# Kernel optimization log

Measured on AMD Instinct MI355X. Metric: run time of the kernel, lower is better.

## Reference

```python
import jax, jax.numpy as jnp
import numpy as np

B, C, Ci, N = 4, 512, 256, 4096
EPS = 1e-5

def _proj(x, W, b):
    # 1x1 Conv1d == per-node linear: x [B,C,N], W [O,C], b [O] -> [B,O,N]
    return jnp.einsum('oc,bcn->bon', W, x) + b[None, :, None]

def setup_inputs() -> dict:
    key = jax.random.key(0)
    ks = jax.random.split(key, 12)
    s_in = 1.0 / np.sqrt(C)
    s_ci = 1.0 / np.sqrt(Ci)
    return {
        'v':   jax.random.normal(ks[0], (B, C, N), jnp.float32),
        'Wg':  jax.random.normal(ks[1], (Ci, C), jnp.float32) * s_in,
        'bg':  jax.random.normal(ks[2], (Ci,), jnp.float32) * 0.01,
        'Wth': jax.random.normal(ks[3], (Ci, C), jnp.float32) * s_in,
        'bth': jax.random.normal(ks[4], (Ci,), jnp.float32) * 0.01,
        'Wph': jax.random.normal(ks[5], (Ci, C), jnp.float32) * s_in,
        'bph': jax.random.normal(ks[6], (Ci,), jnp.float32) * 0.01,
        'Ww':  jax.random.normal(ks[7], (C, Ci), jnp.float32) * s_ci,
        'bw':  jax.random.normal(ks[8], (C,), jnp.float32) * 0.01,
        'gamma': jax.random.uniform(ks[9], (C,), jnp.float32, 0.5, 1.5),
        'beta':  jax.random.normal(ks[10], (C,), jnp.float32) * 0.01,
    }

def reference(v, Wg, bg, Wth, bth, Wph, bph, Ww, bw, gamma, beta):
    # projections (1x1 convs)
    g_v = _proj(v, Wg, bg).transpose(0, 2, 1)      # [B,N,Ci]
    theta_v = _proj(v, Wth, bth).transpose(0, 2, 1)  # [B,N,Ci]
    phi_v = _proj(v, Wph, bph)                      # [B,Ci,N]
    # non-local affinity (no softmax), divided by N
    R = jnp.einsum('bnc,bcm->bnm', theta_v, phi_v) / N  # [B,N,N]
    y = jnp.einsum('bnm,bmc->bnc', R, g_v)              # [B,N,Ci]
    y = y.transpose(0, 2, 1)                            # [B,Ci,N]
    # W: 1x1 conv back to C, then BatchNorm1d (training-mode stats)
    Wy = _proj(y, Ww, bw)                               # [B,C,N]
    mean = jnp.mean(Wy, axis=(0, 2), keepdims=True)
    var = jnp.mean(jnp.square(Wy - mean), axis=(0, 2), keepdims=True)  # biased, as torch BN uses
    Wy_bn = (Wy - mean) * jax.lax.rsqrt(var + EPS)
    Wy_bn = Wy_bn * gamma[None, :, None] + beta[None, :, None]
    return Wy_bn + v
```

## Files before the change

kernel.cpp:

```cpp
#include <hip/hip_runtime.h>
#include <math.h>


#define B_  4
#define C_  512
#define CI_ 256
#define N_  4096

typedef __attribute__((ext_vector_type(8))) short bf16x8;
typedef __attribute__((ext_vector_type(4))) float f32x4;

#define G_OFF     0L
#define P1_OFF    1048576L
#define SP_OFF    1572864L
#define P2_OFF    1835008L
#define MISC_OFF  2359296L
#define R_OFF     (MISC_OFF + 0)
#define SUM_OFF   (MISC_OFF + 2048)
#define SSQ_OFF   (MISC_OFF + 2560)
#define BE_OFF    (MISC_OFF + 3072)
#define U1_OFF    (MISC_OFF + 5120)
#define U2_OFF    (MISC_OFF + 6144)
#define VH_OFF    2367488L
#define VL_OFF    6561792L
#define VTH_OFF   10756096L
#define WEH_OFF   14950400L
#define WEL_OFF   15474688L

__device__ __forceinline__ unsigned short f2bf(float f) {
    union { float f; unsigned int u; } a; a.f = f;
    unsigned int u = a.u;
    u += 0x7fffu + ((u >> 16) & 1u);
    return (unsigned short)(u >> 16);
}
__device__ __forceinline__ float bf2f(unsigned short s) {
    union { unsigned int u; float f; } a; a.u = ((unsigned int)s) << 16; return a.f;
}
__device__ __forceinline__ void gload_lds16(const char* g, char* l) {
    __builtin_amdgcn_global_load_lds(
        (const __attribute__((address_space(1))) unsigned int*)g,
        (__attribute__((address_space(3))) unsigned int*)l, 16, 0, 0);
}

__global__ __launch_bounds__(256) void cast_fused(
    const float* __restrict__ v, unsigned short* __restrict__ vh,
    unsigned short* __restrict__ vl, unsigned short* __restrict__ vth,
    float* __restrict__ r)
{
    __shared__ float tile[64][65];
    const int b = blockIdx.z;
    const int n0 = blockIdx.x * 64, c0 = blockIdx.y * 64;
    const int t = threadIdx.x, rq = t >> 4, cq = t & 15;
#pragma unroll
    for (int p = 0; p < 4; ++p) {
        int row = p * 16 + rq;
        long e = ((long)(b * C_ + c0 + row)) * N_ + n0 + cq * 4;
        float4 f = *(const float4*)&v[e];
        ushort4 h, l;
        h.x = f2bf(f.x); l.x = f2bf(f.x - bf2f(h.x));
        h.y = f2bf(f.y); l.y = f2bf(f.y - bf2f(h.y));
        h.z = f2bf(f.z); l.z = f2bf(f.z - bf2f(h.z));
        h.w = f2bf(f.w); l.w = f2bf(f.w - bf2f(h.w));
        *(ushort4*)&vh[e] = h;
        *(ushort4*)&vl[e] = l;
        tile[row][cq * 4 + 0] = f.x; tile[row][cq * 4 + 1] = f.y;
        tile[row][cq * 4 + 2] = f.z; tile[row][cq * 4 + 3] = f.w;
        float s = f.x + f.y + f.z + f.w;
        s += __shfl_xor(s, 1); s += __shfl_xor(s, 2);
        s += __shfl_xor(s, 4); s += __shfl_xor(s, 8);
        if (cq == 0) atomicAdd(&r[b * C_ + c0 + row], s);
    }
    __syncthreads();
#pragma unroll
    for (int p = 0; p < 4; ++p) {
        int nl = p * 16 + rq;
        float f0 = tile[cq * 4 + 0][nl], f1 = tile[cq * 4 + 1][nl];
        float f2 = tile[cq * 4 + 2][nl], f3 = tile[cq * 4 + 3][nl];
        ushort4 h;
        h.x = f2bf(f0); h.y = f2bf(f1); h.z = f2bf(f2); h.w = f2bf(f3);
        long e = ((long)(b * N_ + n0 + nl)) * C_ + c0 + cq * 4;
        *(ushort4*)&vth[e] = h;
    }
}

__global__ __launch_bounds__(256, 4) void gram_mfma(
    const unsigned short* __restrict__ vh, const unsigned short* __restrict__ vl,
    float* __restrict__ G)
{
    __shared__ char smem[32768];
    const int t = threadIdx.x, lane = t & 63, w = t >> 6;
    const int z = blockIdx.z, b = z >> 3, ch = z & 7;
    const long m0 = blockIdx.y * 128, n0 = blockIdx.x * 64;
    const long k0b = (long)ch * 1024;
    const long stride = (long)N_ * 2;

    const char* g; char* lbase;
    if (w == 0)      { g = (const char*)(vh + ((long)b * C_ + m0     ) * N_) + k0b; lbase = smem; }
    else if (w == 1) { g = (const char*)(vh + ((long)b * C_ + m0 + 64) * N_) + k0b; lbase = smem + 8192; }
    else if (w == 2) { g = (const char*)(vh + ((long)b * C_ + n0     ) * N_) + k0b; lbase = smem + 16384; }
    else             { g = (const char*)(vl + ((long)b * C_ + n0     ) * N_) + k0b; lbase = smem + 24576; }
    const char* gs = g + (long)(lane >> 3) * stride + (((lane & 7) ^ (lane >> 3)) << 4);

    const int wr = w >> 1, wc = w & 1;
    const int l15 = lane & 15, hi4 = lane >> 4;
    const int swz = (l15 & 7) << 4;
    const int arow = (wr * 64 + l15) * 128;
    const int brow = (wc * 32 + l15) * 128;
    const char* Ah = smem;
    const char* Bh = smem + 16384;
    const char* Bl = smem + 24576;

    f32x4 acc[4][2];
#pragma unroll
    for (int mi = 0; mi < 4; ++mi)
#pragma unroll
        for (int nj = 0; nj < 2; ++nj) acc[mi][nj] = (f32x4){0.f, 0.f, 0.f, 0.f};

    for (int s = 0; s < 8; ++s) {
#pragma unroll
        for (int i = 0; i < 8; ++i)
            gload_lds16(gs + (long)i * 8 * stride + s * 128, lbase + i * 1024);
        __syncthreads();
#pragma unroll
        for (int kk = 0; kk < 2; ++kk) {
            const int off = (kk * 64 + hi4 * 16) ^ swz;
            bf16x8 ah[4], bh[2], bl[2];
#pragma unroll
            for (int mi = 0; mi < 4; ++mi)
                ah[mi] = *(const bf16x8*)(Ah + arow + mi * 2048 + off);
#pragma unroll
            for (int nj = 0; nj < 2; ++nj) {
                bh[nj] = *(const bf16x8*)(Bh + brow + nj * 2048 + off);
                bl[nj] = *(const bf16x8*)(Bl + brow + nj * 2048 + off);
            }
#pragma unroll
            for (int mi = 0; mi < 4; ++mi)
#pragma unroll
                for (int nj = 0; nj < 2; ++nj)
                    acc[mi][nj] = __builtin_amdgcn_mfma_f32_16x16x32_bf16(ah[mi], bh[nj], acc[mi][nj], 0, 0, 0);
#pragma unroll
            for (int mi = 0; mi < 4; ++mi)
#pragma unroll
                for (int nj = 0; nj < 2; ++nj)
                    acc[mi][nj] = __builtin_amdgcn_mfma_f32_16x16x32_bf16(ah[mi], bl[nj], acc[mi][nj], 0, 0, 0);
        }
        __syncthreads();
    }
#pragma unroll
    for (int mi = 0; mi < 4; ++mi)
#pragma unroll
        for (int nj = 0; nj < 2; ++nj)
#pragma unroll
            for (int rr = 0; rr < 4; ++rr) {
                long row = m0 + wr * 64 + mi * 16 + hi4 * 4 + rr;
                long col = n0 + wc * 32 + nj * 16 + l15;
                atomicAdd(&G[((long)b * C_ + row) * C_ + col], acc[mi][nj][rr]);
            }
}

__global__ __launch_bounds__(256, 4) void wy_mfma(
    const unsigned short* __restrict__ weh, const unsigned short* __restrict__ wel,
    const unsigned short* __restrict__ vth,
    const float* __restrict__ be, const float* __restrict__ bw,
    float* __restrict__ out, float* __restrict__ sums, float* __restrict__ ssqs)
{
    __shared__ char smem[40960];
    const int t = threadIdx.x, lane = t & 63, w = t >> 6;
    const int b = blockIdx.z;
    const long m0 = blockIdx.y * 128;
    const long n0 = blockIdx.x * 64;
    const long S = (long)C_ * 2;

    const char* wehb = (const char*)(weh + ((long)b * C_ + m0) * C_);
    const char* welb = (const char*)(wel + ((long)b * C_ + m0) * C_);
    const char* vhb  = (const char*)(vth + ((long)b * N_ + n0) * C_);

    const char *g0, *g1; char *l0, *l1; int c0n;
    if (w == 0)      { g0 = wehb;           l0 = smem;                 c0n = 10; g1 = wehb; l1 = smem; }
    else if (w == 1) { g0 = wehb + 80 * S;  l0 = smem + 10240;         c0n = 6;  g1 = welb;          l1 = smem + 16384; }
    else if (w == 2) { g0 = welb + 32 * S;  l0 = smem + 16384 + 4096;  c0n = 10; g1 = welb; l1 = smem + 16384; }
    else             { g0 = welb + 112 * S; l0 = smem + 16384 + 14336; c0n = 2;  g1 = vhb;           l1 = smem + 32768; }
    const long plane = (long)(lane >> 3) * S + (((lane & 7) ^ (lane >> 3)) << 4);

    const int wr = w >> 1, wc = w & 1;
    const int l15 = lane & 15, hi4 = lane >> 4;
    const int swz = (l15 & 7) << 4;
    const int arow = (wr * 64 + l15) * 128;
    const int brow = (wc * 32 + l15) * 128;
    const char* Ah = smem;
    const char* Al = smem + 16384;
    const char* Bv = smem + 32768;

    f32x4 acc[4][2];
#pragma unroll
    for (int mi = 0; mi < 4; ++mi)
#pragma unroll
        for (int nj = 0; nj < 2; ++nj) acc[mi][nj] = (f32x4){0.f, 0.f, 0.f, 0.f};

    for (int s = 0; s < 8; ++s) {
#pragma unroll
        for (int i = 0; i < 10; ++i) {
            const char* src; char* dst;
            if (i < c0n) { src = g0 + (long)i * 8 * S;         dst = l0 + i * 1024; }
            else         { src = g1 + (long)(i - c0n) * 8 * S; dst = l1 + (i - c0n) * 1024; }
            gload_lds16(src + plane + s * 128, dst);
        }
        __syncthreads();
#pragma unroll
        for (int kk = 0; kk < 2; ++kk) {
            const int off = (kk * 64 + hi4 * 16) ^ swz;
            bf16x8 ah[4], al[4], bv[2];
#pragma unroll
            for (int mi = 0; mi < 4; ++mi) {
                ah[mi] = *(const bf16x8*)(Ah + arow + mi * 2048 + off);
                al[mi] = *(const bf16x8*)(Al + arow + mi * 2048 + off);
            }
#pragma unroll
            for (int nj = 0; nj < 2; ++nj)
                bv[nj] = *(const bf16x8*)(Bv + brow + nj * 2048 + off);
#pragma unroll
            for (int mi = 0; mi < 4; ++mi)
#pragma unroll
                for (int nj = 0; nj < 2; ++nj)
                    acc[mi][nj] = __builtin_amdgcn_mfma_f32_16x16x32_bf16(ah[mi], bv[nj], acc[mi][nj], 0, 0, 0);
#pragma unroll
            for (int mi = 0; mi < 4; ++mi)
#pragma unroll
                for (int nj = 0; nj < 2; ++nj)
                    acc[mi][nj] = __builtin_amdgcn_mfma_f32_16x16x32_bf16(al[mi], bv[nj], acc[mi][nj], 0, 0, 0);
        }
        __syncthreads();
    }

    float sm[4][4], sq[4][4];
#pragma unroll
    for (int mi = 0; mi < 4; ++mi)
#pragma unroll
        for (int rr = 0; rr < 4; ++rr) { sm[mi][rr] = 0.f; sq[mi][rr] = 0.f; }

#pragma unroll
    for (int mi = 0; mi < 4; ++mi) {
#pragma unroll
        for (int rr = 0; rr < 4; ++rr) {
            long o = m0 + wr * 64 + mi * 16 + hi4 * 4 + rr;
            float bv = be[b * C_ + o] * (1.0f / (float)N_) + bw[o];
#pragma unroll
            for (int nj = 0; nj < 2; ++nj) {
                long n = n0 + wc * 32 + nj * 16 + l15;
                float val = acc[mi][nj][rr] + bv;
                out[((long)b * C_ + o) * N_ + n] = val;
                sm[mi][rr] += val;
                sq[mi][rr] += val * val;
            }
        }
    }
#pragma unroll
    for (int mi = 0; mi < 4; ++mi)
#pragma unroll
        for (int rr = 0; rr < 4; ++rr) {
            float s1 = sm[mi][rr], s2 = sq[mi][rr];
            s1 += __shfl_xor(s1, 1); s2 += __shfl_xor(s2, 1);
            s1 += __shfl_xor(s1, 2); s2 += __shfl_xor(s2, 2);
            s1 += __shfl_xor(s1, 4); s2 += __shfl_xor(s2, 4);
            s1 += __shfl_xor(s1, 8); s2 += __shfl_xor(s2, 8);
            if (l15 == 0) {
                long o = m0 + wr * 64 + mi * 16 + hi4 * 4 + rr;
                atomicAdd(&sums[o], s1);
                atomicAdd(&ssqs[o], s2);
            }
        }
}

__global__ __launch_bounds__(256) void gemm_nn(
    const float* __restrict__ A, long sA, int lda,
    const float* __restrict__ Bm, long sB, int ldb,
    float* __restrict__ Cm, long sC, int ldc,
    int K, float scale, int mode,
    const float* __restrict__ bth, float* __restrict__ be,
    unsigned short* __restrict__ weh, unsigned short* __restrict__ wel)
{
    int b = blockIdx.z;
    const float* Ab = A + (long)b * sA;
    const float* Bb = Bm + (long)b * sB;
    int i0 = blockIdx.y * 64, j0 = blockIdx.x * 64;

    __shared__ __align__(16) float As[16][64];
    __shared__ __align__(16) float Bs[16][64];

    int t = threadIdx.x, tx = t & 15, ty = t >> 4;
    int am = t >> 2, akq = (t & 3) << 2;
    int bk = t >> 4, bn4 = (t & 15) << 2;

    float acc[4][4];
#pragma unroll
    for (int r = 0; r < 4; ++r)
#pragma unroll
        for (int c = 0; c < 4; ++c) acc[r][c] = 0.f;

    for (int k0 = 0; k0 < K; k0 += 16) {
        float4 va = *(const float4*)&Ab[(long)(i0 + am) * lda + k0 + akq];
        As[akq + 0][am] = va.x; As[akq + 1][am] = va.y;
        As[akq + 2][am] = va.z; As[akq + 3][am] = va.w;
        *(float4*)&Bs[bk][bn4] = *(const float4*)&Bb[(long)(k0 + bk) * ldb + j0 + bn4];
        __syncthreads();
#pragma unroll
        for (int k = 0; k < 16; ++k) {
            float4 a4 = *(float4*)&As[k][ty * 4];
            float4 b4 = *(float4*)&Bs[k][tx * 4];
            float a[4]  = {a4.x, a4.y, a4.z, a4.w};
            float bb[4] = {b4.x, b4.y, b4.z, b4.w};
#pragma unroll
            for (int r = 0; r < 4; ++r)
#pragma unroll
                for (int c = 0; c < 4; ++c)
                    acc[r][c] += a[r] * bb[c];
        }
        __syncthreads();
    }

    if (mode == 2) {
#pragma unroll
        for (int r = 0; r < 4; ++r) {
            int o = i0 + ty * 4 + r, p = j0 + tx * 4;
            ushort4 h, l;
            float f0 = acc[r][0] * scale, f1 = acc[r][1] * scale;
            float f2 = acc[r][2] * scale, f3 = acc[r][3] * scale;
            h.x = f2bf(f0); l.x = f2bf(f0 - bf2f(h.x));
            h.y = f2bf(f1); l.y = f2bf(f1 - bf2f(h.y));
            h.z = f2bf(f2); l.z = f2bf(f2 - bf2f(h.z));
            h.w = f2bf(f3); l.w = f2bf(f3 - bf2f(h.w));
            long e = (((long)b * C_ + o) * C_ + p) >> 2;
            ((ushort4*)weh)[e] = h;
            ((ushort4*)wel)[e] = l;
        }
        return;
    }
    float* Cb = Cm + (long)b * sC;
#pragma unroll
    for (int r = 0; r < 4; ++r) {
        float4 o0 = make_float4(acc[r][0] * scale, acc[r][1] * scale,
                                acc[r][2] * scale, acc[r][3] * scale);
        *(float4*)&Cb[(long)(i0 + ty * 4 + r) * ldc + j0 + tx * 4] = o0;
    }
    if (mode == 1) {
#pragma unroll
        for (int r = 0; r < 4; ++r) {
            float pr = acc[r][0] * bth[j0 + tx * 4 + 0]
                     + acc[r][1] * bth[j0 + tx * 4 + 1]
                     + acc[r][2] * bth[j0 + tx * 4 + 2]
                     + acc[r][3] * bth[j0 + tx * 4 + 3];
            pr += __shfl_xor(pr, 1); pr += __shfl_xor(pr, 2);
            pr += __shfl_xor(pr, 4); pr += __shfl_xor(pr, 8);
            if (tx == 0) atomicAdd(&be[b * C_ + i0 + ty * 4 + r], pr);
        }
    }
}

__global__ __launch_bounds__(256) void gemm_nt_sp(
    const float* __restrict__ P1, const float* __restrict__ Wph,
    float* __restrict__ SP, const float* __restrict__ u1,
    const float* __restrict__ u2, const float* __restrict__ bg,
    const float* __restrict__ bph)
{
    int b = blockIdx.z;
    const float* Ab = P1 + (long)b * (CI_ * C_);
    int i0 = blockIdx.y * 64, j0 = blockIdx.x * 64;

    __shared__ __align__(16) float As[16][64];
    __shared__ __align__(16) float Bs[16][64];

    int t = threadIdx.x, tx = t & 15, ty = t >> 4;
    int lr = t >> 2, lk = (t & 3) << 2;

    float acc[4][4];
#pragma unroll
    for (int r = 0; r < 4; ++r)
#pragma unroll
        for (int c = 0; c < 4; ++c) acc[r][c] = 0.f;

    for (int kt = 0; kt < C_; kt += 16) {
        float4 va = *(const float4*)&Ab[(long)(i0 + lr) * C_ + kt + lk];
        float4 vb = *(const float4*)&Wph[(long)(j0 + lr) * C_ + kt + lk];
        As[lk + 0][lr] = va.x; As[lk + 1][lr] = va.y; As[lk + 2][lr] = va.z; As[lk + 3][lr] = va.w;
        Bs[lk + 0][lr] = vb.x; Bs[lk + 1][lr] = vb.y; Bs[lk + 2][lr] = vb.z; Bs[lk + 3][lr] = vb.w;
        __syncthreads();
#pragma unroll
        for (int k = 0; k < 16; ++k) {
            float4 a4 = *(float4*)&As[k][ty * 4];
            float4 b4 = *(float4*)&Bs[k][tx * 4];
            float a[4]  = {a4.x, a4.y, a4.z, a4.w};
            float bb[4] = {b4.x, b4.y, b4.z, b4.w};
#pragma unroll
            for (int r = 0; r < 4; ++r)
#pragma unroll
                for (int c = 0; c < 4; ++c)
                    acc[r][c] += a[r] * bb[c];
        }
        __syncthreads();
    }
    float* Cb = SP + (long)b * (CI_ * CI_);
#pragma unroll
    for (int r = 0; r < 4; ++r) {
        int cr = i0 + ty * 4 + r;
        float u1v = u1[b * CI_ + cr], bgv = bg[cr];
        float4 o0;
        float* po = (float*)&o0;
#pragma unroll
        for (int c = 0; c < 4; ++c) {
            int ic = j0 + tx * 4 + c;
            po[c] = acc[r][c] + u1v * bph[ic] + bgv * (u2[b * CI_ + ic] + (float)N_ * bph[ic]);
        }
        *(float4*)&Cb[(long)cr * CI_ + j0 + tx * 4] = o0;
    }
}

__global__ __launch_bounds__(256) void rank1_prep(
    const float* __restrict__ Wg, const float* __restrict__ Wph,
    const float* __restrict__ r, float* __restrict__ u1, float* __restrict__ u2)
{
    int blk = blockIdx.x;
    int b = blk >> 2, q = blk & 3;
    int t = threadIdx.x;
    int c = q * 64 + (t >> 2);
    int kq = t & 3;
    const float* rb = r + b * C_;
    float s1 = 0.f, s2 = 0.f;
    for (int k = kq * 128; k < kq * 128 + 128; k += 4) {
        float4 wg = *(const float4*)&Wg[(long)c * C_ + k];
        float4 wp = *(const float4*)&Wph[(long)c * C_ + k];
        float4 rv = *(const float4*)&rb[k];
        s1 += wg.x * rv.x + wg.y * rv.y + wg.z * rv.z + wg.w * rv.w;
        s2 += wp.x * rv.x + wp.y * rv.y + wp.z * rv.z + wp.w * rv.w;
    }
    s1 += __shfl_xor(s1, 1); s2 += __shfl_xor(s2, 1);
    s1 += __shfl_xor(s1, 2); s2 += __shfl_xor(s2, 2);
    if (kq == 0) {
        u1[b * CI_ + c] = s1;
        u2[b * CI_ + c] = s2;
    }
}

__global__ __launch_bounds__(256) void bn_apply(
    float* __restrict__ out, const float* __restrict__ v,
    const float* __restrict__ sums, const float* __restrict__ ssqs,
    const float* __restrict__ gamma, const float* __restrict__ beta)
{
    long i = (long)blockIdx.x * 256 + threadIdx.x;
    int o = (int)((i >> 10) & (C_ - 1));
    const float inv = 1.0f / ((float)B_ * (float)N_);
    float mean = sums[o] * inv;
    float var  = ssqs[o] * inv - mean * mean;
    float sc = gamma[o] * rsqrtf(var + 1e-5f);
    float sh = beta[o] - mean * sc;
    float4 wv = ((const float4*)out)[i];
    float4 vv = ((const float4*)v)[i];
    wv.x = wv.x * sc + sh + vv.x;
    wv.y = wv.y * sc + sh + vv.y;
    wv.z = wv.z * sc + sh + vv.z;
    wv.w = wv.w * sc + sh + vv.w;
    ((float4*)out)[i] = wv;
}

extern "C" void kernel_launch(void* const* d_in, const int* in_sizes, int n_in,
                              void* d_out, int out_size, void* d_ws, size_t ws_size,
                              hipStream_t stream)
{
    const float* v     = (const float*)d_in[0];
    const float* Wg    = (const float*)d_in[1];
    const float* bg    = (const float*)d_in[2];
    const float* Wth   = (const float*)d_in[3];
    const float* bth   = (const float*)d_in[4];
    const float* Wph   = (const float*)d_in[5];
    const float* bph   = (const float*)d_in[6];
    const float* Ww    = (const float*)d_in[7];
    const float* bw    = (const float*)d_in[8];
    const float* gamma = (const float*)d_in[9];
    const float* beta  = (const float*)d_in[10];
    float* out = (float*)d_out;
    float* ws  = (float*)d_ws;

    float* G    = ws + G_OFF;
    float* P1   = ws + P1_OFF;
    float* SP   = ws + SP_OFF;
    float* P2   = ws + P2_OFF;
    float* r    = ws + R_OFF;
    float* sums = ws + SUM_OFF;
    float* ssqs = ws + SSQ_OFF;
    float* be   = ws + BE_OFF;
    float* u1   = ws + U1_OFF;
    float* u2   = ws + U2_OFF;
    unsigned short* vh  = (unsigned short*)(ws + VH_OFF);
    unsigned short* vl  = (unsigned short*)(ws + VL_OFF);
    unsigned short* vth = (unsigned short*)(ws + VTH_OFF);
    unsigned short* weh = (unsigned short*)(ws + WEH_OFF);
    unsigned short* wel = (unsigned short*)(ws + WEL_OFF);

    hipMemsetAsync(G, 0, 1048576 * sizeof(float), stream);
    hipMemsetAsync(r, 0, 5120 * sizeof(float), stream);

    cast_fused<<<dim3(64, 8, 4), 256, 0, stream>>>(v, vh, vl, vth, r);

    gram_mfma<<<dim3(8, 4, 32), 256, 0, stream>>>(vh, vl, G);

    rank1_prep<<<16, 256, 0, stream>>>(Wg, Wph, r, u1, u2);

    gemm_nn<<<dim3(8, 4, 4), 256, 0, stream>>>(
        Wg, 0, C_, G, (long)C_ * C_, C_, P1, (long)CI_ * C_, C_,
        C_, 1.0f, 0, nullptr, nullptr, nullptr, nullptr);

    gemm_nt_sp<<<dim3(4, 4, 4), 256, 0, stream>>>(P1, Wph, SP, u1, u2, bg, bph);

    gemm_nn<<<dim3(4, 8, 4), 256, 0, stream>>>(
        Ww, 0, CI_, SP, (long)CI_ * CI_, CI_, P2, (long)C_ * CI_, CI_,
        CI_, 1.0f, 1, bth, be, nullptr, nullptr);

    gemm_nn<<<dim3(8, 8, 4), 256, 0, stream>>>(
        P2, (long)C_ * CI_, CI_, Wth, 0, C_, nullptr, 0, 0,
        CI_, 1.0f / (float)N_, 2, nullptr, nullptr, weh, wel);

    wy_mfma<<<dim3(64, 4, 4), 256, 0, stream>>>(weh, wel, vth, be, bw, out, sums, ssqs);

    bn_apply<<<8192, 256, 0, stream>>>(out, v, sums, ssqs, gamma, beta);
}
```

Before: 344.7 us.

## Compute BN stats analytically from Gram matrix and fuse BN apply into Wy GEMM

BatchNorm statistics are now derived algebraically from the Gram matrix G = v v^T: a small GEMM H = W_eff G plus row dot products give the per-channel sum of squares, so the large output no longer has to be written, reread and normalized in a separate bn_apply pass. The Wy GEMM applies scale, shift and the residual directly in its epilogue. The Gram kernel exploits symmetry by computing only upper-triangular 128x128 tiles, with a mirror kernel filling in the rest. Tiles grow to 128x128 at lower occupancy. The cost is several extra small kernels and a bf16-cast G, which may reduce the accuracy of the variance.

```diff
diff --git a/kernel.cpp b/kernel.cpp
--- a/kernel.cpp
+++ b/kernel.cpp
@@ -11,21 +11,25 @@
 typedef __attribute__((ext_vector_type(4))) float f32x4;
 
 #define G_OFF     0L
-#define P1_OFF    1048576L
-#define SP_OFF    1572864L
-#define P2_OFF    1835008L
-#define MISC_OFF  2359296L
+#define GH_OFF    1048576L
+#define H_OFF     1572864L
+#define P1_OFF    2621440L
+#define SP_OFF    3145728L
+#define P2_OFF    3407872L
+#define MISC_OFF  3932160L
 #define R_OFF     (MISC_OFF + 0)
-#define SUM_OFF   (MISC_OFF + 2048)
-#define SSQ_OFF   (MISC_OFF + 2560)
-#define BE_OFF    (MISC_OFF + 3072)
-#define U1_OFF    (MISC_OFF + 5120)
-#define U2_OFF    (MISC_OFF + 6144)
-#define VH_OFF    2367488L
-#define VL_OFF    6561792L
-#define VTH_OFF   10756096L
-#define WEH_OFF   14950400L
-#define WEL_OFF   15474688L
+#define BE_OFF    (MISC_OFF + 2048)
+#define U1_OFF    (MISC_OFF + 4096)
+#define U2_OFF    (MISC_OFF + 5120)
+#define QF_OFF    (MISC_OFF + 6144)
+#define MV_OFF    (MISC_OFF + 8192)
+#define SC_OFF    (MISC_OFF + 10240)
+#define SH_OFF    (MISC_OFF + 10752)
+#define VH_OFF    3944448L
+#define VL_OFF    8138752L
+#define VTH_OFF   12333056L
+#define WEH_OFF   16527360L
+#define WEL_OFF   17051648L
 
 __device__ __forceinline__ unsigned short f2bf(float f) {
     union { float f; unsigned int u; } a; a.f = f;
@@ -83,65 +87,73 @@
     }
 }
 
-__global__ __launch_bounds__(256, 4) void gram_mfma(
+__global__ __launch_bounds__(256, 2) void gram_mfma(
     const unsigned short* __restrict__ vh, const unsigned short* __restrict__ vl,
     float* __restrict__ G)
 {
-    __shared__ char smem[32768];
+    __shared__ char smem[49152];
+    const int MT[10] = {0,1,1,2,2,2,3,3,3,3};
+    const int NT[10] = {0,0,1,0,1,2,0,1,2,3};
     const int t = threadIdx.x, lane = t & 63, w = t >> 6;
-    const int z = blockIdx.z, b = z >> 3, ch = z & 7;
-    const long m0 = blockIdx.y * 128, n0 = blockIdx.x * 64;
-    const long k0b = (long)ch * 1024;
+    const int z = blockIdx.z, b = z >> 4, ch = z & 15;
+    const long m0 = MT[blockIdx.x] * 128, n0 = NT[blockIdx.x] * 128;
+    const long k0b = (long)ch * 512;
     const long stride = (long)N_ * 2;
 
-    const char* g; char* lbase;
-    if (w == 0)      { g = (const char*)(vh + ((long)b * C_ + m0     ) * N_) + k0b; lbase = smem; }
-    else if (w == 1) { g = (const char*)(vh + ((long)b * C_ + m0 + 64) * N_) + k0b; lbase = smem + 8192; }
-    else if (w == 2) { g = (const char*)(vh + ((long)b * C_ + n0     ) * N_) + k0b; lbase = smem + 16384; }
-    else             { g = (const char*)(vl + ((long)b * C_ + n0     ) * N_) + k0b; lbase = smem + 24576; }
-    const char* gs = g + (long)(lane >> 3) * stride + (((lane & 7) ^ (lane >> 3)) << 4);
+    const char* vhm = (const char*)(vh + ((long)b * C_ + m0) * N_) + k0b;
+    const char* vhn = (const char*)(vh + ((long)b * C_ + n0) * N_) + k0b;
+    const char* vln = (const char*)(vl + ((long)b * C_ + n0) * N_) + k0b;
+    char* AhL = smem; char* BhL = smem + 16384; char* BlL = smem + 32768;
+
+    const char *g0, *g1; char *l0, *l1; int c0n;
+    if (w == 0)      { g0 = vhm;                l0 = AhL;             c0n = 12; g1 = g0;  l1 = l0; }
+    else if (w == 1) { g0 = vhm + 96 * stride;  l0 = AhL + 12 * 1024; c0n = 4;  g1 = vhn; l1 = BhL; }
+    else if (w == 2) { g0 = vhn + 64 * stride;  l0 = BhL + 8 * 1024;  c0n = 8;  g1 = vln; l1 = BlL; }
+    else             { g0 = vln + 32 * stride;  l0 = BlL + 4 * 1024;  c0n = 12; g1 = g0;  l1 = l0; }
+    const long plane = (long)(lane >> 3) * stride + (((lane & 7) ^ (lane >> 3)) << 4);
 
     const int wr = w >> 1, wc = w & 1;
     const int l15 = lane & 15, hi4 = lane >> 4;
     const int swz = (l15 & 7) << 4;
     const int arow = (wr * 64 + l15) * 128;
-    const int brow = (wc * 32 + l15) * 128;
-    const char* Ah = smem;
-    const char* Bh = smem + 16384;
-    const char* Bl = smem + 24576;
-
-    f32x4 acc[4][2];
+    const int brow = (wc * 64 + l15) * 128;
+
+    f32x4 acc[4][4];
 #pragma unroll
     for (int mi = 0; mi < 4; ++mi)
 #pragma unroll
-        for (int nj = 0; nj < 2; ++nj) acc[mi][nj] = (f32x4){0.f, 0.f, 0.f, 0.f};
-
-    for (int s = 0; s < 8; ++s) {
-#pragma unroll
-        for (int i = 0; i < 8; ++i)
-            gload_lds16(gs + (long)i * 8 * stride + s * 128, lbase + i * 1024);
+        for (int nj = 0; nj < 4; ++nj) acc[mi][nj] = (f32x4){0.f, 0.f, 0.f, 0.f};
+
+    for (int s = 0; s < 4; ++s) {
+#pragma unroll
+        for (int i = 0; i < 12; ++i) {
+            const char* src; char* dst;
+            if (i < c0n) { src = g0 + (long)i * 8 * stride;         dst = l0 + i * 1024; }
+            else         { src = g1 + (long)(i - c0n) * 8 * stride; dst = l1 + (i - c0n) * 1024; }
+            gload_lds16(src + plane + s * 128, dst);
+        }
         __syncthreads();
 #pragma unroll
         for (int kk = 0; kk < 2; ++kk) {
             const int off = (kk * 64 + hi4 * 16) ^ swz;
-            bf16x8 ah[4], bh[2], bl[2];
+            bf16x8 ah[4], bh[4], bl[4];
 #pragma unroll
             for (int mi = 0; mi < 4; ++mi)
-                ah[mi] = *(const bf16x8*)(Ah + arow + mi * 2048 + off);
-#pragma unroll
-            for (int nj = 0; nj < 2; ++nj) {
-                bh[nj] = *(const bf16x8*)(Bh + brow + nj * 2048 + off);
-                bl[nj] = *(const bf16x8*)(Bl + brow + nj * 2048 + off);
+                ah[mi] = *(const bf16x8*)(AhL + arow + mi * 2048 + off);
+#pragma unroll
+            for (int nj = 0; nj < 4; ++nj) {
+                bh[nj] = *(const bf16x8*)(BhL + brow + nj * 2048 + off);
+                bl[nj] = *(const bf16x8*)(BlL + brow + nj * 2048 + off);
             }
 #pragma unroll
             for (int mi = 0; mi < 4; ++mi)
 #pragma unroll
-                for (int nj = 0; nj < 2; ++nj)
+                for (int nj = 0; nj < 4; ++nj)
                     acc[mi][nj] = __builtin_amdgcn_mfma_f32_16x16x32_bf16(ah[mi], bh[nj], acc[mi][nj], 0, 0, 0);
 #pragma unroll
             for (int mi = 0; mi < 4; ++mi)
 #pragma unroll
-                for (int nj = 0; nj < 2; ++nj)
+                for (int nj = 0; nj < 4; ++nj)
                     acc[mi][nj] = __builtin_amdgcn_mfma_f32_16x16x32_bf16(ah[mi], bl[nj], acc[mi][nj], 0, 0, 0);
         }
         __syncthreads();
@@ -149,57 +161,98 @@
 #pragma unroll
     for (int mi = 0; mi < 4; ++mi)
 #pragma unroll
-        for (int nj = 0; nj < 2; ++nj)
+        for (int nj = 0; nj < 4; ++nj)
 #pragma unroll
             for (int rr = 0; rr < 4; ++rr) {
                 long row = m0 + wr * 64 + mi * 16 + hi4 * 4 + rr;
-                long col = n0 + wc * 32 + nj * 16 + l15;
+                long col = n0 + wc * 64 + nj * 16 + l15;
                 atomicAdd(&G[((long)b * C_ + row) * C_ + col], acc[mi][nj][rr]);
             }
 }
 
-__global__ __launch_bounds__(256, 4) void wy_mfma(
+__global__ __launch_bounds__(256) void mirror_g(float* __restrict__ G)
+{
+    const int J = blockIdx.x, I = blockIdx.y, b = blockIdx.z;
+    if (I > J) return;
+    __shared__ float tile[64][65];
+    const int t = threadIdx.x, ty = t >> 4, tx = t & 15;
+    float* Gb = G + (long)b * C_ * C_;
+#pragma unroll
+    for (int p = 0; p < 4; ++p) {
+        int row = p * 16 + ty;
+        *(float4*)&tile[row][tx * 4] =
+            *(const float4*)&Gb[(long)(J * 64 + row) * C_ + I * 64 + tx * 4];
+    }
+    __syncthreads();
+    if (I < J) {
+#pragma unroll
+        for (int p = 0; p < 4; ++p) {
+            int row = p * 16 + ty;
+            float4 o = make_float4(tile[tx * 4 + 0][row], tile[tx * 4 + 1][row],
+                                   tile[tx * 4 + 2][row], tile[tx * 4 + 3][row]);
+            *(float4*)&Gb[(long)(I * 64 + row) * C_ + J * 64 + tx * 4] = o;
+        }
+    } else {
+#pragma unroll
+        for (int p = 0; p < 4; ++p) {
+            int row = p * 16 + ty;
+            int i = I * 64 + row;
+#pragma unroll
+            for (int c = 0; c < 4; ++c) {
+                int j = J * 64 + tx * 4 + c;
+                if (i < j) Gb[(long)i * C_ + j] = tile[tx * 4 + c][row];
+            }
+        }
+    }
+}
+
+__global__ __launch_bounds__(256) void g_cast(
+    const float* __restrict__ G, unsigned short* __restrict__ Gh)
+{
+    long idx = (long)blockIdx.x * 256 + threadIdx.x;
+    float4 f = ((const float4*)G)[idx];
+    ushort4 h;
+    h.x = f2bf(f.x); h.y = f2bf(f.y); h.z = f2bf(f.z); h.w = f2bf(f.w);
+    ((ushort4*)Gh)[idx] = h;
+}
+
+__global__ __launch_bounds__(256, 2) void h_mfma(
     const unsigned short* __restrict__ weh, const unsigned short* __restrict__ wel,
-    const unsigned short* __restrict__ vth,
-    const float* __restrict__ be, const float* __restrict__ bw,
-    float* __restrict__ out, float* __restrict__ sums, float* __restrict__ ssqs)
-{
-    __shared__ char smem[40960];
+    const unsigned short* __restrict__ Gh, float* __restrict__ H)
+{
+    __shared__ char smem[49152];
     const int t = threadIdx.x, lane = t & 63, w = t >> 6;
     const int b = blockIdx.z;
-    const long m0 = blockIdx.y * 128;
-    const long n0 = blockIdx.x * 64;
+    const long m0 = blockIdx.y * 128, n0 = blockIdx.x * 128;
     const long S = (long)C_ * 2;
 
     const char* wehb = (const char*)(weh + ((long)b * C_ + m0) * C_);
     const char* welb = (const char*)(wel + ((long)b * C_ + m0) * C_);
-    const char* vhb  = (const char*)(vth + ((long)b * N_ + n0) * C_);
+    const char* ghb  = (const char*)(Gh  + ((long)b * C_ + n0) * C_);
+    char* AhL = smem; char* AlL = smem + 16384; char* BhL = smem + 32768;
 
     const char *g0, *g1; char *l0, *l1; int c0n;
-    if (w == 0)      { g0 = wehb;           l0 = smem;                 c0n = 10; g1 = wehb; l1 = smem; }
-    else if (w == 1) { g0 = wehb + 80 * S;  l0 = smem + 10240;         c0n = 6;  g1 = welb;          l1 = smem + 16384; }
-    else if (w == 2) { g0 = welb + 32 * S;  l0 = smem + 16384 + 4096;  c0n = 10; g1 = welb; l1 = smem + 16384; }
-    else             { g0 = welb + 112 * S; l0 = smem + 16384 + 14336; c0n = 2;  g1 = vhb;           l1 = smem + 32768; }
+    if (w == 0)      { g0 = wehb;          l0 = AhL;             c0n = 12; g1 = g0;   l1 = l0; }
+    else if (w == 1) { g0 = wehb + 96 * S; l0 = AhL + 12 * 1024; c0n = 4;  g1 = welb; l1 = AlL; }
+    else if (w == 2) { g0 = welb + 64 * S; l0 = AlL + 8 * 1024;  c0n = 8;  g1 = ghb;  l1 = BhL; }
+    else             { g0 = ghb + 32 * S;  l0 = BhL + 4 * 1024;  c0n = 12; g1 = g0;   l1 = l0; }
     const long plane = (long)(lane >> 3) * S + (((lane & 7) ^ (lane >> 3)) << 4);
 
     const int wr = w >> 1, wc = w & 1;
     const int l15 = lane & 15, hi4 = lane >> 4;
     const int swz = (l15 & 7) << 4;
     const int arow = (wr * 64 + l15) * 128;
-    const int brow = (wc * 32 + l15) * 128;
-    const char* Ah = smem;
-    const char* Al = smem + 16384;
-    const char* Bv = smem + 32768;
-
-    f32x4 acc[4][2];
+    const int brow = (wc * 64 + l15) * 128;
+
+    f32x4 acc[4][4];
 #pragma unroll
     for (int mi = 0; mi < 4; ++mi)
 #pragma unroll
-        for (int nj = 0; nj < 2; ++nj) acc[mi][nj] = (f32x4){0.f, 0.f, 0.f, 0.f};
+        for (int nj = 0; nj < 4; ++nj) acc[mi][nj] = (f32x4){0.f, 0.f, 0.f, 0.f};
 
     for (int s = 0; s < 8; ++s) {
 #pragma unroll
-        for (int i = 0; i < 10; ++i) {
+        for (int i = 0; i < 12; ++i) {
             const char* src; char* dst;
             if (i < c0n) { src = g0 + (long)i * 8 * S;         dst = l0 + i * 1024; }
             else         { src = g1 + (long)(i - c0n) * 8 * S; dst = l1 + (i - c0n) * 1024; }
@@ -209,66 +262,185 @@
 #pragma unroll
         for (int kk = 0; kk < 2; ++kk) {
             const int off = (kk * 64 + hi4 * 16) ^ swz;
-            bf16x8 ah[4], al[4], bv[2];
+            bf16x8 ah[4], al[4], bh[4];
 #pragma unroll
             for (int mi = 0; mi < 4; ++mi) {
-                ah[mi] = *(const bf16x8*)(Ah + arow + mi * 2048 + off);
-                al[mi] = *(const bf16x8*)(Al + arow + mi * 2048 + off);
+                ah[mi] = *(const bf16x8*)(AhL + arow + mi * 2048 + off);
+                al[mi] = *(const bf16x8*)(AlL + arow + mi * 2048 + off);
             }
 #pragma unroll
-            for (int nj = 0; nj < 2; ++nj)
-                bv[nj] = *(const bf16x8*)(Bv + brow + nj * 2048 + off);
+            for (int nj = 0; nj < 4; ++nj)
+                bh[nj] = *(const bf16x8*)(BhL + brow + nj * 2048 + off);
 #pragma unroll
             for (int mi = 0; mi < 4; ++mi)
 #pragma unroll
-                for (int nj = 0; nj < 2; ++nj)
-                    acc[mi][nj] = __builtin_amdgcn_mfma_f32_16x16x32_bf16(ah[mi], bv[nj], acc[mi][nj], 0, 0, 0);
+                for (int nj = 0; nj < 4; ++nj)
+                    acc[mi][nj] = __builtin_amdgcn_mfma_f32_16x16x32_bf16(ah[mi], bh[nj], acc[mi][nj], 0, 0, 0);
 #pragma unroll
             for (int mi = 0; mi < 4; ++mi)
 #pragma unroll
-                for (int nj = 0; nj < 2; ++nj)
-                    acc[mi][nj] = __builtin_amdgcn_mfma_f32_16x16x32_bf16(al[mi], bv[nj], acc[mi][nj], 0, 0, 0);
-        }
-        __syncthreads();
-    }
-
-    float sm[4][4], sq[4][4];
+                for (int nj = 0; nj < 4; ++nj)
+                    acc[mi][nj] = __builtin_amdgcn_mfma_f32_16x16x32_bf16(al[mi], bh[nj], acc[mi][nj], 0, 0, 0);
+        }
+        __syncthreads();
+    }
 #pragma unroll
     for (int mi = 0; mi < 4; ++mi)
 #pragma unroll
-        for (int rr = 0; rr < 4; ++rr) { sm[mi][rr] = 0.f; sq[mi][rr] = 0.f; }
+        for (int nj = 0; nj < 4; ++nj)
+#pragma unroll
+            for (int rr = 0; rr < 4; ++rr) {
+                long row = m0 + wr * 64 + mi * 16 + hi4 * 4 + rr;
+                long col = n0 + wc * 64 + nj * 16 + l15;
+                H[((long)b * C_ + row) * C_ + col] = acc[mi][nj][rr];
+            }
+}
+
+__global__ __launch_bounds__(256) void stats_k(
+    const float* __restrict__ H, const unsigned short* __restrict__ weh,
+    const unsigned short* __restrict__ wel, const float* __restrict__ r,
+    float* __restrict__ QF, float* __restrict__ MV)
+{
+    const int bo = blockIdx.x;
+    const int b = bo >> 9;
+    const float* Hr = H + (long)bo * C_;
+    const unsigned short* wh = weh + (long)bo * C_;
+    const unsigned short* wl = wel + (long)bo * C_;
+    const float* rb = r + b * C_;
+    const int t = threadIdx.x;
+    float qf = 0.f, mv = 0.f;
+    for (int j = t; j < C_; j += 256) {
+        float ws = bf2f(wh[j]) + bf2f(wl[j]);
+        qf += Hr[j] * ws;
+        mv += ws * rb[j];
+    }
+    qf += __shfl_xor(qf, 1);  mv += __shfl_xor(mv, 1);
+    qf += __shfl_xor(qf, 2);  mv += __shfl_xor(mv, 2);
+    qf += __shfl_xor(qf, 4);  mv += __shfl_xor(mv, 4);
+    qf += __shfl_xor(qf, 8);  mv += __shfl_xor(mv, 8);
+    qf += __shfl_xor(qf, 16); mv += __shfl_xor(mv, 16);
+    qf += __shfl_xor(qf, 32); mv += __shfl_xor(mv, 32);
+    __shared__ float sq[4], sm[4];
+    if ((t & 63) == 0) { sq[t >> 6] = qf; sm[t >> 6] = mv; }
+    __syncthreads();
+    if (t == 0) {
+        QF[bo] = sq[0] + sq[1] + sq[2] + sq[3];
+        MV[bo] = sm[0] + sm[1] + sm[2] + sm[3];
+    }
+}
+
+__global__ __launch_bounds__(512) void finalize_k(
+    const float* __restrict__ QF, const float* __restrict__ MV,
+    const float* __restrict__ be, const float* __restrict__ bw,
+    const float* __restrict__ gamma, const float* __restrict__ beta,
+    float* __restrict__ sc, float* __restrict__ sh)
+{
+    int o = threadIdx.x;
+    float mean_acc = 0.f, ssq = 0.f;
+    for (int b = 0; b < B_; ++b) {
+        float bf = be[b * C_ + o] * (1.0f / (float)N_) + bw[o];
+        float m = MV[b * C_ + o];
+        float q = QF[b * C_ + o];
+        mean_acc += m + (float)N_ * bf;
+        ssq += q + 2.0f * bf * m + (float)N_ * bf * bf;
+    }
+    const float inv = 1.0f / ((float)B_ * (float)N_);
+    float mean = mean_acc * inv;
+    float var = ssq * inv - mean * mean;
+    float s = gamma[o] * rsqrtf(var + 1e-5f);
+    sc[o] = s;
+    sh[o] = beta[o] - mean * s;
+}
+
+__global__ __launch_bounds__(256, 2) void wy_mfma(
+    const unsigned short* __restrict__ weh, const unsigned short* __restrict__ wel,
+    const unsigned short* __restrict__ vth,
+    const float* __restrict__ be, const float* __restrict__ bw,
+    const float* __restrict__ sc, const float* __restrict__ sh,
+    const float* __restrict__ v, float* __restrict__ out)
+{
+    __shared__ char smem[49152];
+    const int t = threadIdx.x, lane = t & 63, w = t >> 6;
+    const int b = blockIdx.z;
+    const long m0 = blockIdx.y * 128;
+    const long n0 = blockIdx.x * 128;
+    const long S = (long)C_ * 2;
+
+    const char* wehb = (const char*)(weh + ((long)b * C_ + m0) * C_);
+    const char* welb = (const char*)(wel + ((long)b * C_ + m0) * C_);
+    const char* vhb  = (const char*)(vth + ((long)b * N_ + n0) * C_);
+    char* AhL = smem; char* AlL = smem + 16384; char* BhL = smem + 32768;
+
+    const char *g0, *g1; char *l0, *l1; int c0n;
+    if (w == 0)      { g0 = wehb;          l0 = AhL;             c0n = 12; g1 = g0;   l1 = l0; }
+    else if (w == 1) { g0 = wehb + 96 * S; l0 = AhL + 12 * 1024; c0n = 4;  g1 = welb; l1 = AlL; }
+    else if (w == 2) { g0 = welb + 64 * S; l0 = AlL + 8 * 1024;  c0n = 8;  g1 = vhb;  l1 = BhL; }
+    else             { g0 = vhb + 32 * S;  l0 = BhL + 4 * 1024;  c0n = 12; g1 = g0;   l1 = l0; }
+    const long plane = (long)(lane >> 3) * S + (((lane & 7) ^ (lane >> 3)) << 4);
+
+    const int wr = w >> 1, wc = w & 1;
+    const int l15 = lane & 15, hi4 = lane >> 4;
+    const int swz = (l15 & 7) << 4;
+    const int arow = (wr * 64 + l15) * 128;
+    const int brow = (wc * 64 + l15) * 128;
+
+    f32x4 acc[4][4];
+#pragma unroll
+    for (int mi = 0; mi < 4; ++mi)
+#pragma unroll
+        for (int nj = 0; nj < 4; ++nj) acc[mi][nj] = (f32x4){0.f, 0.f, 0.f, 0.f};
+
+    for (int s = 0; s < 8; ++s) {
+#pragma unroll
+        for (int i = 0; i < 12; ++i) {
+            const char* src; char* dst;
+            if (i < c0n) { src = g0 + (long)i * 8 * S;         dst = l0 + i * 1024; }
+            else         { src = g1 + (long)(i - c0n) * 8 * S; dst = l1 + (i - c0n) * 1024; }
+            gload_lds16(src + plane + s * 128, dst);
+        }
+        __syncthreads();
+#pragma unroll
+        for (int kk = 0; kk < 2; ++kk) {
+            const int off = (kk * 64 + hi4 * 16) ^ swz;
+            bf16x8 ah[4], al[4], bh[4];
+#pragma unroll
+            for (int mi = 0; mi < 4; ++mi) {
+                ah[mi] = *(const bf16x8*)(AhL + arow + mi * 2048 + off);
+                al[mi] = *(const bf16x8*)(AlL + arow + mi * 2048 + off);
+            }
+#pragma unroll
+            for (int nj = 0; nj < 4; ++nj)
+                bh[nj] = *(const bf16x8*)(BhL + brow + nj * 2048 + off);
+#pragma unroll
+            for (int mi = 0; mi < 4; ++mi)
+#pragma unroll
+                for (int nj = 0; nj < 4; ++nj)
+                    acc[mi][nj] = __builtin_amdgcn_mfma_f32_16x16x32_bf16(ah[mi], bh[nj], acc[mi][nj], 0, 0, 0);
+#pragma unroll
+            for (int mi = 0; mi < 4; ++mi)
+#pragma unroll
+                for (int nj = 0; nj < 4; ++nj)
+                    acc[mi][nj] = __builtin_amdgcn_mfma_f32_16x16x32_bf16(al[mi], bh[nj], acc[mi][nj], 0, 0, 0);
+        }
+        __syncthreads();
+    }
 
 #pragma unroll
     for (int mi = 0; mi < 4; ++mi) {
 #pragma unroll
         for (int rr = 0; rr < 4; ++rr) {
             long o = m0 + wr * 64 + mi * 16 + hi4 * 4 + rr;
-            float bv = be[b * C_ + o] * (1.0f / (float)N_) + bw[o];
-#pragma unroll
-            for (int nj = 0; nj < 2; ++nj) {
-                long n = n0 + wc * 32 + nj * 16 + l15;
-                float val = acc[mi][nj][rr] + bv;
-                out[((long)b * C_ + o) * N_ + n] = val;
-                sm[mi][rr] += val;
-                sq[mi][rr] += val * val;
+            float bf = be[b * C_ + o] * (1.0f / (float)N_) + bw[o];
+            float s_c = sc[o], s_h = sh[o];
+#pragma unroll
+            for (int nj = 0; nj < 4; ++nj) {
+                long n = n0 + wc * 64 + nj * 16 + l15;
+                long e = ((long)b * C_ + o) * N_ + n;
+                float val = acc[mi][nj][rr] + bf;
+                out[e] = val * s_c + s_h + v[e];
             }
         }
     }
-#pragma unroll
-    for (int mi = 0; mi < 4; ++mi)
-#pragma unroll
-        for (int rr = 0; rr < 4; ++rr) {
-            float s1 = sm[mi][rr], s2 = sq[mi][rr];
-            s1 += __shfl_xor(s1, 1); s2 += __shfl_xor(s2, 1);
-            s1 += __shfl_xor(s1, 2); s2 += __shfl_xor(s2, 2);
-            s1 += __shfl_xor(s1, 4); s2 += __shfl_xor(s2, 4);
-            s1 += __shfl_xor(s1, 8); s2 += __shfl_xor(s2, 8);
-            if (l15 == 0) {
-                long o = m0 + wr * 64 + mi * 16 + hi4 * 4 + rr;
-                atomicAdd(&sums[o], s1);
-                atomicAdd(&ssqs[o], s2);
-            }
-        }
 }
 
 __global__ __launch_bounds__(256) void gemm_nn(
@@ -440,27 +612,6 @@
     }
 }
 
-__global__ __launch_bounds__(256) void bn_apply(
-    float* __restrict__ out, const float* __restrict__ v,
-    const float* __restrict__ sums, const float* __restrict__ ssqs,
-    const float* __restrict__ gamma, const float* __restrict__ beta)
-{
-    long i = (long)blockIdx.x * 256 + threadIdx.x;
-    int o = (int)((i >> 10) & (C_ - 1));
-    const float inv = 1.0f / ((float)B_ * (float)N_);
-    float mean = sums[o] * inv;
-    float var  = ssqs[o] * inv - mean * mean;
-    float sc = gamma[o] * rsqrtf(var + 1e-5f);
-    float sh = beta[o] - mean * sc;
-    float4 wv = ((const float4*)out)[i];
-    float4 vv = ((const float4*)v)[i];
-    wv.x = wv.x * sc + sh + vv.x;
-    wv.y = wv.y * sc + sh + vv.y;
-    wv.z = wv.z * sc + sh + vv.z;
-    wv.w = wv.w * sc + sh + vv.w;
-    ((float4*)out)[i] = wv;
-}
-
 extern "C" void kernel_launch(void* const* d_in, const int* in_sizes, int n_in,
                               void* d_out, int out_size, void* d_ws, size_t ws_size,
                               hipStream_t stream)
@@ -480,15 +631,19 @@
     float* ws  = (float*)d_ws;
 
     float* G    = ws + G_OFF;
+    float* H    = ws + H_OFF;
     float* P1   = ws + P1_OFF;
     float* SP   = ws + SP_OFF;
     float* P2   = ws + P2_OFF;
     float* r    = ws + R_OFF;
-    float* sums = ws + SUM_OFF;
-    float* ssqs = ws + SSQ_OFF;
     float* be   = ws + BE_OFF;
     float* u1   = ws + U1_OFF;
     float* u2   = ws + U2_OFF;
+    float* QF   = ws + QF_OFF;
+    float* MV   = ws + MV_OFF;
+    float* sc   = ws + SC_OFF;
+    float* sh   = ws + SH_OFF;
+    unsigned short* Gh  = (unsigned short*)(ws + GH_OFF);
     unsigned short* vh  = (unsigned short*)(ws + VH_OFF);
     unsigned short* vl  = (unsigned short*)(ws + VL_OFF);
     unsigned short* vth = (unsigned short*)(ws + VTH_OFF);
@@ -496,11 +651,12 @@
     unsigned short* wel = (unsigned short*)(ws + WEL_OFF);
 
     hipMemsetAsync(G, 0, 1048576 * sizeof(float), stream);
-    hipMemsetAsync(r, 0, 5120 * sizeof(float), stream);
+    hipMemsetAsync(r, 0, 4096 * sizeof(float), stream);
 
     cast_fused<<<dim3(64, 8, 4), 256, 0, stream>>>(v, vh, vl, vth, r);
 
-    gram_mfma<<<dim3(8, 4, 32), 256, 0, stream>>>(vh, vl, G);
+    gram_mfma<<<dim3(10, 1, 64), 256, 0, stream>>>(vh, vl, G);
+    mirror_g<<<dim3(8, 8, 4), 256, 0, stream>>>(G);
 
     rank1_prep<<<16, 256, 0, stream>>>(Wg, Wph, r, u1, u2);
 
@@ -518,7 +674,10 @@
         P2, (long)C_ * CI_, CI_, Wth, 0, C_, nullptr, 0, 0,
         CI_, 1.0f / (float)N_, 2, nullptr, nullptr, weh, wel);
 
-    wy_mfma<<<dim3(64, 4, 4), 256, 0, stream>>>(weh, wel, vth, be, bw, out, sums, ssqs);
-
-    bn_apply<<<8192, 256, 0, stream>>>(out, v, sums, ssqs, gamma, beta);
-}
+    g_cast<<<1024, 256, 0, stream>>>(G, Gh);
+    h_mfma<<<dim3(4, 4, 4), 256, 0, stream>>>(weh, wel, Gh, H);
+    stats_k<<<2048, 256, 0, stream>>>(H, weh, wel, r, QF, MV);
+    finalize_k<<<1, 512, 0, stream>>>(QF, MV, be, bw, gamma, beta, sc, sh);
+
+    wy_mfma<<<dim3(32, 4, 4), 256, 0, stream>>>(weh, wel, vth, be, bw, sc, sh, v, out);
+}
```

New measurement: 309.8 us. 1.11x faster.
